# Kernel tuning notes

Measured on AMD Instinct MI355X. Metric: run time of the kernel, lower is better.

## Reference

```python
import jax, jax.numpy as jnp
from jax import lax
import numpy as np

VAR0, VAR1 = 0.1, 0.2
K_TOP, T1, T2 = 5, 0.35, 0.5
ALPHA, GAMMA, BETA = 0.25, 2.0, 0.11


def point_form(b):
    # center form (cx,cy,w,h) -> corner form (x1,y1,x2,y2)
    return jnp.concatenate([b[:, :2] - b[:, 2:] / 2, b[:, :2] + b[:, 2:] / 2], axis=-1)


def jaccard(a, b):
    # a: [N,4], b: [P,4] corner boxes -> IoU [N,P]
    lt = jnp.maximum(a[:, None, :2], b[None, :, :2])
    rb = jnp.minimum(a[:, None, 2:], b[None, :, 2:])
    wh = jnp.clip(rb - lt, 0.0)
    inter = wh[..., 0] * wh[..., 1]
    area_a = ((a[:, 2] - a[:, 0]) * (a[:, 3] - a[:, 1]))[:, None]
    area_b = ((b[:, 2] - b[:, 0]) * (b[:, 3] - b[:, 1]))[None, :]
    return inter / (area_a + area_b - inter)


def encode(matched, priors):
    # matched: corner boxes [P,4], priors: center form [P,4]
    g_cxcy = ((matched[:, :2] + matched[:, 2:]) / 2 - priors[:, :2]) / (VAR0 * priors[:, 2:])
    g_wh = jnp.log((matched[:, 2:] - matched[:, :2]) / priors[:, 2:]) / VAR1
    return jnp.concatenate([g_cxcy, g_wh], axis=-1)


def decode(loc, priors):
    cxcy = priors[:, :2] + loc[:, :2] * VAR0 * priors[:, 2:]
    wh = priors[:, 2:] * jnp.exp(loc[:, 2:] * VAR1)
    return jnp.concatenate([cxcy - wh / 2, cxcy + wh / 2], axis=-1)


def _bce_logits(x, t):
    return jnp.maximum(x, 0.0) - x * t + jnp.log1p(jnp.exp(-jnp.abs(x)))


def focal_loss(logits, target, f_iou=None):
    C = logits.shape[-1]
    t = target.reshape(-1, 1)
    keep = (t >= 0.0).astype(logits.dtype)
    t = jnp.maximum(t, 0.0)
    pos = jnp.sum(t > 0.0).astype(logits.dtype)
    x = jnp.take_along_axis(logits.reshape(-1, C), t.astype(jnp.int32), axis=1)
    ce = _bce_logits(x, t)
    a = t * ALPHA + (1.0 - t) * (1.0 - ALPHA)
    p = jax.nn.sigmoid(x)
    pt = jnp.where(t == 1.0, p, 1.0 - p)
    if f_iou is not None:
        a = lax.stop_gradient(f_iou.reshape(-1, 1)) * a
    loss = a * (1.0 - pt) ** GAMMA * ce * keep
    return jnp.sum(loss) / jnp.maximum(pos, 1.0)


def smoothl1_masked(pred, target, mask):
    # equals SmoothL1Loss on the masked rows: sum(elem)/num_rows
    x = jnp.abs(pred - target)
    elem = jnp.where(x >= BETA, x - 0.5 * BETA, 0.5 * x * x / BETA)
    n = jnp.sum(mask).astype(pred.dtype)
    return jnp.sum(elem * mask[..., None].astype(pred.dtype)) / jnp.maximum(n, 1.0)


def match_image(loc_pred, tgt, priors_c, priors_pt):
    N = tgt.shape[0]
    P = priors_c.shape[0]
    truths = tgt[:, :4]
    labels = tgt[:, 4]
    iou = jaccard(truths, priors_pt)  # [N,P]
    bt_score = jnp.max(iou, axis=0)
    bt_idx = jnp.argmax(iou, axis=0).astype(jnp.int32)

    def greedy(_, st):
        m, s, ix = st
        flat = jnp.argmax(m)
        j = (flat // P).astype(jnp.int32)
        i = (flat % P).astype(jnp.int32)
        v = m.ravel()[flat]
        m = m.at[j, :].set(-1.0)
        m = m.at[:, i].set(-1.0)
        return (m, s.at[i].set(v), ix.at[i].set(j))

    _, bt_score, bt_idx = lax.fori_loop(0, N, greedy, (iou, bt_score, bt_idx))

    conf_s1 = labels[bt_idx]
    conf_s1 = jnp.where(bt_score < T1, 0.0, conf_s1)
    loc_s1 = encode(truths[bt_idx], priors_c)

    decoded = decode(lax.stop_gradient(loc_pred), priors_c)
    c_iou = jaccard(truths, decoded)  # [N,P]
    c_bp_score = jnp.max(c_iou, axis=0)
    c_bp_idx = jnp.argmax(c_iou, axis=0).astype(jnp.int32)
    c_iou = c_iou * (c_iou >= T2).astype(c_iou.dtype)
    tk_s, tk_i = lax.top_k(c_iou, K_TOP)  # per-truth top-K priors
    c_score = jnp.zeros_like(c_bp_score)

    def assign(t, st):
        cbi, cs = st
        i = (t // K_TOP).astype(jnp.int32)
        j = t % K_TOP
        p = tk_i[i, j]
        s = tk_s[i, j]
        cond = (conf_s1[p] < 1.0) & (s > 0.0)
        cbi = cbi.at[p].set(jnp.where(cond, i, cbi[p]))
        cs = cs.at[p].set(jnp.where(cond, s, cs[p]))
        return (cbi, cs)

    c_bp_idx, c_score = lax.fori_loop(0, N * K_TOP, assign, (c_bp_idx, c_score))

    loc_s2 = encode(truths[c_bp_idx], priors_c)
    conf_s2 = labels[c_bp_idx]
    conf_s2 = jnp.where(c_score < T2, -1.0, conf_s2)
    ignore = (bt_score < T1) & (c_bp_score >= T2) & (c_score < T2)
    conf_s1 = jnp.where(ignore, -1.0, conf_s1)
    return conf_s1, loc_s1, conf_s2, loc_s2, c_score


def setup_inputs() -> dict:
    key = jax.random.key(0)
    k1, k2, k3, k4, k5, k6 = jax.random.split(key, 6)
    B, P, N, C = 16, 102400, 32, 2
    loc_data = jax.random.normal(k1, (B, P, 4), jnp.float32)
    conf_data = jax.random.normal(k2, (B, P, C), jnp.float32)
    pcxy = jax.random.uniform(k3, (P, 2), jnp.float32, 0.0, 1.0)
    pwh = jax.random.uniform(k4, (P, 2), jnp.float32, 0.02, 0.25)
    priors = jnp.concatenate([pcxy, pwh], axis=-1)
    tcxy = jax.random.uniform(k5, (B, N, 2), jnp.float32, 0.1, 0.9)
    twh = jax.random.uniform(k6, (B, N, 2), jnp.float32, 0.05, 0.3)
    x1 = jnp.clip(tcxy - twh / 2, 0.0, 1.0)
    x2 = jnp.clip(tcxy + twh / 2, 0.0, 1.0)
    targets = jnp.concatenate([x1, x2, jnp.ones((B, N, 1), jnp.float32)], axis=-1)
    return {"loc_data": loc_data, "conf_data": conf_data, "priors": priors, "targets": targets}


def reference(loc_data, conf_data, priors, targets):
    priors_c = lax.stop_gradient(priors)  # torch uses priors.data
    tgts = lax.stop_gradient(targets)     # torch uses targets[idx].data
    priors_pt = point_form(priors_c)
    conf_t, loc_t, cconf_t, cloc_t, cc_score = jax.vmap(
        lambda lp, tg: match_image(lp, tg, priors_c, priors_pt))(loc_data, tgts)
    m1 = conf_t > 0.0
    m2 = cconf_t > 0.0
    n1 = jnp.sum(m1)
    n2 = jnp.sum(m2)
    l1 = smoothl1_masked(loc_data, loc_t, m1)
    l2 = smoothl1_masked(loc_data, cloc_t, m2)
    f1 = focal_loss(conf_data, conf_t, None)
    f2 = focal_loss(conf_data, cconf_t, cc_score)
    loc_loss = jnp.where(n1 > 0, l1, 0.0) + jnp.where(n2 > 0, l2, 0.0)
    cls_loss = jnp.where(n1 > 0, f1, 0.0) + jnp.where(n2 > 0, f2, 0.0)
    none_ = (n1 == 0) & (n2 == 0)
    return (jnp.where(none_, 1e-4, loc_loss), jnp.where(none_, 1e-4, cls_loss))
```

## Files before the change

### kernel.cpp

```cpp
#include <hip/hip_runtime.h>
#include <cstdint>
#include <cstddef>

#define VAR0_ 0.1f
#define VAR1_ 0.2f
#define KTOP_ 5
#define T1_ 0.35f
#define T2_ 0.5f
#define ALPHA_ 0.25f
#define BETA_ 0.11f
#define BS 256
#define RSPLIT 8
#define ILP 4

__device__ __forceinline__ float sl1(float d) {
    float x = fabsf(d);
    return (x >= BETA_) ? (x - 0.5f * BETA_) : (0.5f * x * x / BETA_);
}

__global__ void k_init(int* __restrict__ cand_cnt, int nCnt) {
    int i = blockIdx.x * blockDim.x + threadIdx.x;
    if (i < nCnt) cand_cnt[i] = 0;
}

__global__ void k_per_prior(const float4* __restrict__ loc4, const float4* __restrict__ priors4,
                            const float* __restrict__ targets,
                            float4* __restrict__ recs4,
                            float* __restrict__ cand_v, int* __restrict__ cand_i,
                            int* __restrict__ cand_cnt,
                            int P, int N, int CAP) {
    int b = blockIdx.y;
    int tid = threadIdx.x;
    int base = blockIdx.x * (BS * ILP) + tid;
    __shared__ float4 tr4[64];
    __shared__ float trA[64];
    __shared__ float trT[64];
    for (int t = tid; t < N; t += BS) {
        float x1 = targets[(size_t)(b * N + t) * 5 + 0];
        float y1 = targets[(size_t)(b * N + t) * 5 + 1];
        float x2 = targets[(size_t)(b * N + t) * 5 + 2];
        float y2 = targets[(size_t)(b * N + t) * 5 + 3];
        tr4[t] = make_float4(x1, y1, x2, y2);
        float a = (x2 - x1) * (y2 - y1);
        trA[t] = a;
        trT[t] = a * 0.33330f;
    }
    __syncthreads();
    if (base >= P) return;

    int iv[ILP]; int val[ILP];
    float px1[ILP], py1[ILP], px2[ILP], py2[ILP], pa[ILP];
#pragma unroll
    for (int k = 0; k < ILP; k++) {
        int i = base + k * BS; iv[k] = i; val[k] = (i < P);
        float4 pr = val[k] ? priors4[i] : make_float4(0.f, 0.f, 1.f, 1.f);
        px1[k] = pr.x - pr.z * 0.5f; py1[k] = pr.y - pr.w * 0.5f;
        px2[k] = pr.x + pr.z * 0.5f; py2[k] = pr.y + pr.w * 0.5f;
        pa[k] = (px2[k] - px1[k]) * (py2[k] - py1[k]);
    }

    float bi[ILP], bu[ILP]; int bn[ILP];
#pragma unroll
    for (int k = 0; k < ILP; k++) { bi[k] = -1.f; bu[k] = 1.f; bn[k] = 0; }
#pragma unroll 2
    for (int n = 0; n < N; n++) {
        float4 t4 = tr4[n];
        float ta = trA[n];
#pragma unroll
        for (int k = 0; k < ILP; k++) {
            float lx = fmaxf(t4.x, px1[k]), ly = fmaxf(t4.y, py1[k]);
            float rx = fminf(t4.z, px2[k]), ry = fminf(t4.w, py2[k]);
            float w = fmaxf(rx - lx, 0.f), h = fmaxf(ry - ly, 0.f);
            float inter = w * h, uni = ta + pa[k] - inter;
            bool bet = inter * bu[k] > bi[k] * uni;
            bi[k] = bet ? inter : bi[k]; bu[k] = bet ? uni : bu[k]; bn[k] = bet ? n : bn[k];
        }
    }
    float bv[ILP];
#pragma unroll
    for (int k = 0; k < ILP; k++) bv[k] = bi[k] / bu[k];

    float dx1[ILP], dy1[ILP], dx2[ILP], dy2[ILP], da[ILP], daC[ILP];
#pragma unroll
    for (int k = 0; k < ILP; k++) {
        float4 pr = val[k] ? priors4[iv[k]] : make_float4(0.f, 0.f, 1.f, 1.f);
        float4 lc = val[k] ? loc4[(size_t)b * P + iv[k]] : make_float4(0.f, 0.f, 0.f, 0.f);
        float dcx = pr.x + lc.x * VAR0_ * pr.z;
        float dcy = pr.y + lc.y * VAR0_ * pr.w;
        float dw = pr.z * expf(lc.z * VAR1_);
        float dh = pr.w * expf(lc.w * VAR1_);
        dx1[k] = dcx - dw * 0.5f; dy1[k] = dcy - dh * 0.5f;
        dx2[k] = dcx + dw * 0.5f; dy2[k] = dcy + dh * 0.5f;
        da[k] = (dx2[k] - dx1[k]) * (dy2[k] - dy1[k]);
        daC[k] = da[k] * 0.33330f;
    }
    unsigned long long hm[ILP];
#pragma unroll
    for (int k = 0; k < ILP; k++) hm[k] = 0ull;
#pragma unroll 2
    for (int n = 0; n < N; n++) {
        float4 t4 = tr4[n];
        float tt = trT[n];
#pragma unroll
        for (int k = 0; k < ILP; k++) {
            float lx = fmaxf(t4.x, dx1[k]), ly = fmaxf(t4.y, dy1[k]);
            float rx = fminf(t4.z, dx2[k]), ry = fminf(t4.w, dy2[k]);
            float w = fmaxf(rx - lx, 0.f), h = fmaxf(ry - ly, 0.f);
            float inter = w * h;
            if (inter >= tt + daC[k]) hm[k] |= (1ull << n);
        }
    }

#pragma unroll
    for (int k = 0; k < ILP; k++) {
        if (!val[k]) continue;
        int had = 0;
        unsigned long long m = hm[k];
        while (m) {
            int n = __ffsll((long long)m) - 1;
            m &= m - 1;
            float4 t4 = tr4[n];
            float lx = fmaxf(t4.x, dx1[k]), ly = fmaxf(t4.y, dy1[k]);
            float rx = fminf(t4.z, dx2[k]), ry = fminf(t4.w, dy2[k]);
            float w = fmaxf(rx - lx, 0.f), h = fmaxf(ry - ly, 0.f);
            float inter = w * h;
            float v = inter / (trA[n] + da[k] - inter);
            if (v >= T2_) {
                had = 1;
                int pos = atomicAdd(&cand_cnt[b * N + n], 1);
                if (pos < CAP) {
                    size_t o = (size_t)(b * N + n) * CAP + pos;
                    cand_v[o] = v; cand_i[o] = iv[k];
                }
            }
        }
        recs4[(size_t)b * P + iv[k]] =
            make_float4(bv[k], __int_as_float(bn[k] | (had << 16)), __int_as_float(0), 0.f);
    }
}

__global__ void k_row_max_part(const float4* __restrict__ priors4, const float* __restrict__ targets,
                               float* __restrict__ part_max, int* __restrict__ part_arg,
                               int P, int N) {
    int n = blockIdx.x, b = blockIdx.y, s = blockIdx.z;
    int chunk = (P + RSPLIT - 1) / RSPLIT;
    int i0 = s * chunk;
    int i1 = min(P, i0 + chunk);
    float tx1 = targets[(size_t)(b * N + n) * 5 + 0];
    float ty1 = targets[(size_t)(b * N + n) * 5 + 1];
    float tx2 = targets[(size_t)(b * N + n) * 5 + 2];
    float ty2 = targets[(size_t)(b * N + n) * 5 + 3];
    float ta = (tx2 - tx1) * (ty2 - ty1);
    float cI[4], cU[4]; int cX[4];
#pragma unroll
    for (int k = 0; k < 4; k++) { cI[k] = -1.f; cU[k] = 1.f; cX[k] = 0x7fffffff; }
    int i = i0 + threadIdx.x;
    for (; i + 3 * BS < i1; i += 4 * BS) {
#pragma unroll
        for (int k = 0; k < 4; k++) {
            int j = i + k * BS;
            float4 pr = priors4[j];
            float px1 = pr.x - pr.z * 0.5f, py1 = pr.y - pr.w * 0.5f;
            float px2 = pr.x + pr.z * 0.5f, py2 = pr.y + pr.w * 0.5f;
            float lx = fmaxf(tx1, px1), ly = fmaxf(ty1, py1);
            float rx = fminf(tx2, px2), ry = fminf(ty2, py2);
            float w = fmaxf(rx - lx, 0.f), h = fmaxf(ry - ly, 0.f);
            float inter = w * h;
            float uni = ta + (px2 - px1) * (py2 - py1) - inter;
            bool bet = inter * cU[k] > cI[k] * uni;
            cI[k] = bet ? inter : cI[k]; cU[k] = bet ? uni : cU[k]; cX[k] = bet ? j : cX[k];
        }
    }
    for (; i < i1; i += BS) {
        float4 pr = priors4[i];
        float px1 = pr.x - pr.z * 0.5f, py1 = pr.y - pr.w * 0.5f;
        float px2 = pr.x + pr.z * 0.5f, py2 = pr.y + pr.w * 0.5f;
        float lx = fmaxf(tx1, px1), ly = fmaxf(ty1, py1);
        float rx = fminf(tx2, px2), ry = fminf(ty2, py2);
        float w = fmaxf(rx - lx, 0.f), h = fmaxf(ry - ly, 0.f);
        float inter = w * h;
        float uni = ta + (px2 - px1) * (py2 - py1) - inter;
        bool bet = inter * cU[0] > cI[0] * uni;
        cI[0] = bet ? inter : cI[0]; cU[0] = bet ? uni : cU[0]; cX[0] = bet ? i : cX[0];
    }
#pragma unroll
    for (int k = 1; k < 4; k++) {
        float l = cI[k] * cU[0], r = cI[0] * cU[k];
        bool bet = (l > r) || ((l == r) && (cX[k] < cX[0]));
        cI[0] = bet ? cI[k] : cI[0]; cU[0] = bet ? cU[k] : cU[0]; cX[0] = bet ? cX[k] : cX[0];
    }
    float bv = cI[0] / cU[0];
    int bx = cX[0];
    int tid = threadIdx.x;
    int lane = tid & 63, wid = tid >> 6;
#pragma unroll
    for (int off = 32; off > 0; off >>= 1) {
        float ov = __shfl_xor(bv, off);
        int oi = __shfl_xor(bx, off);
        if (ov > bv || (ov == bv && oi < bx)) { bv = ov; bx = oi; }
    }
    __shared__ float swv[BS / 64];
    __shared__ int swi[BS / 64];
    if (lane == 0) { swv[wid] = bv; swi[wid] = bx; }
    __syncthreads();
    if (tid == 0) {
        float fv = swv[0]; int fi = swi[0];
        for (int wv = 1; wv < BS / 64; wv++) {
            if (swv[wv] > fv || (swv[wv] == fv && swi[wv] < fi)) { fv = swv[wv]; fi = swi[wv]; }
        }
        int o = (b * N + n) * RSPLIT + s;
        part_max[o] = fv; part_arg[o] = fi;
    }
}

__global__ void k_greedy(const float4* __restrict__ priors4, const float* __restrict__ targets,
                         const float* __restrict__ part_max, const int* __restrict__ part_arg,
                         float* __restrict__ recs, int P, int N) {
    int b = blockIdx.x;
    int lane = threadIdx.x;
    extern __shared__ unsigned int mask[];
    int maskWords = (P + 31) >> 5;
    for (int w = lane; w < maskWords; w += 64) mask[w] = 0u;

    float rmax = -2.f; int rarg = 0x7fffffff; int alive = 0;
    float tx1 = 0.f, ty1 = 0.f, tx2 = 0.f, ty2 = 0.f, ta = 0.f;
    if (lane < N) {
        float bv = -2.f; int bi = 0x7fffffff;
        for (int s = 0; s < RSPLIT; s++) {
            int o = (b * N + lane) * RSPLIT + s;
            float v = part_max[o]; int ix = part_arg[o];
            if (v > bv || (v == bv && ix < bi)) { bv = v; bi = ix; }
        }
        rmax = bv; rarg = bi;
        alive = 1;
        tx1 = targets[(size_t)(b * N + lane) * 5 + 0];
        ty1 = targets[(size_t)(b * N + lane) * 5 + 1];
        tx2 = targets[(size_t)(b * N + lane) * 5 + 2];
        ty2 = targets[(size_t)(b * N + lane) * 5 + 3];
        ta = (tx2 - tx1) * (ty2 - ty1);
    }
    __syncthreads();

    for (int it = 0; it < N; it++) {
        float v = (lane < N && alive) ? rmax : -3.f;
        int idx = lane;
#pragma unroll
        for (int off = 32; off > 0; off >>= 1) {
            float ov = __shfl_xor(v, off);
            int oi = __shfl_xor(idx, off);
            if (ov > v || (ov == v && oi < idx)) { v = ov; idx = oi; }
        }
        int bj = idx;
        float bv = v;
        int sel = __shfl(rarg, bj);
        if (lane == bj) alive = 0;
        if (lane == 0) {
            float* base = recs + 4 * ((size_t)b * P + sel);
            int wrd = __float_as_int(base[1]);
            base[0] = bv;
            base[1] = __int_as_float((wrd & ~0xFFFF) | bj);
            mask[sel >> 5] |= (1u << (sel & 31));
        }
        __syncthreads();

        unsigned long long coll = __ballot(lane < N && alive && rarg == sel);
        while (coll) {
            int r = __ffsll((long long)coll) - 1;
            coll &= coll - 1;
            float rx1 = __shfl(tx1, r), ry1 = __shfl(ty1, r);
            float rx2 = __shfl(tx2, r), ry2 = __shfl(ty2, r);
            float ra = __shfl(ta, r);
            float n_i = -2.f, n_u = 1.f; int ni = 0x7fffffff;
            for (int i = lane; i < P; i += 64) {
                if (mask[i >> 5] & (1u << (i & 31))) continue;
                float4 pr = priors4[i];
                float px1 = pr.x - pr.z * 0.5f, py1 = pr.y - pr.w * 0.5f;
                float px2 = pr.x + pr.z * 0.5f, py2 = pr.y + pr.w * 0.5f;
                float lx = fmaxf(rx1, px1), ly = fmaxf(ry1, py1);
                float rx = fminf(rx2, px2), ry = fminf(ry2, py2);
                float w = fmaxf(rx - lx, 0.f), h = fmaxf(ry - ly, 0.f);
                float inter = w * h;
                float uni = ra + (px2 - px1) * (py2 - py1) - inter;
                bool better = inter * n_u > n_i * uni;
                n_i = better ? inter : n_i; n_u = better ? uni : n_u; ni = better ? i : ni;
            }
            float nv = n_i / n_u;
#pragma unroll
            for (int off = 32; off > 0; off >>= 1) {
                float ov = __shfl_xor(nv, off);
                int oi = __shfl_xor(ni, off);
                if (ov > nv || (ov == nv && oi < ni)) { nv = ov; ni = oi; }
            }
            if (lane == r) { rmax = nv; rarg = ni; }
        }
        __syncthreads();
    }
}

__global__ void k_topk(const float4* __restrict__ loc4, const float4* __restrict__ priors4,
                       const float* __restrict__ targets,
                       const float* __restrict__ cand_v, const int* __restrict__ cand_i,
                       const int* __restrict__ cand_cnt,
                       float* __restrict__ tk_s, int* __restrict__ tk_i,
                       int P, int N, int CAP) {
    int n = blockIdx.x, b = blockIdx.y;
    int row = b * N + n;
    int tid = threadIdx.x;

    float vals[KTOP_]; int ids[KTOP_];
#pragma unroll
    for (int k = 0; k < KTOP_; k++) { vals[k] = -1.f; ids[k] = 0x7fffffff; }

    int cnt = cand_cnt[row];
    if (cnt <= CAP) {
        for (int k = tid; k < cnt; k += blockDim.x) {
            float cv = cand_v[(size_t)row * CAP + k];
            int ci = cand_i[(size_t)row * CAP + k];
#pragma unroll
            for (int q = 0; q < KTOP_; q++) {
                bool better = (cv > vals[q]) || ((cv == vals[q]) && (ci < ids[q]));
                float tv = better ? cv : vals[q]; int ti = better ? ci : ids[q];
                cv = better ? vals[q] : cv; ci = better ? ids[q] : ci;
                vals[q] = tv; ids[q] = ti;
            }
        }
    } else {
        float tx1 = targets[(size_t)row * 5 + 0], ty1 = targets[(size_t)row * 5 + 1];
        float tx2 = targets[(size_t)row * 5 + 2], ty2 = targets[(size_t)row * 5 + 3];
        float ta = (tx2 - tx1) * (ty2 - ty1);
        for (int i = tid; i < P; i += blockDim.x) {
            float4 pr = priors4[i];
            size_t bp = (size_t)b * P + i;
            float4 lc = loc4[bp];
            float dcx = pr.x + lc.x * VAR0_ * pr.z;
            float dcy = pr.y + lc.y * VAR0_ * pr.w;
            float dw = pr.z * expf(lc.z * VAR1_);
            float dh = pr.w * expf(lc.w * VAR1_);
            float dx1 = dcx - dw * 0.5f, dy1 = dcy - dh * 0.5f;
            float dx2 = dcx + dw * 0.5f, dy2 = dcy + dh * 0.5f;
            float lx = fmaxf(tx1, dx1), ly = fmaxf(ty1, dy1);
            float rx = fminf(tx2, dx2), ry = fminf(ty2, dy2);
            float w = fmaxf(rx - lx, 0.f), h = fmaxf(ry - ly, 0.f);
            float inter = w * h;
            float uni = ta + (dx2 - dx1) * (dy2 - dy1) - inter;
            if (inter >= uni * 0.4999990f) {
                float v = inter / uni;
                if (v >= T2_) {
                    float cv = v; int ci = i;
#pragma unroll
                    for (int q = 0; q < KTOP_; q++) {
                        bool better = (cv > vals[q]) || ((cv == vals[q]) && (ci < ids[q]));
                        float tv = better ? cv : vals[q]; int ti = better ? ci : ids[q];
                        cv = better ? vals[q] : cv; ci = better ? ids[q] : ci;
                        vals[q] = tv; ids[q] = ti;
                    }
                }
            }
        }
    }

    __shared__ float mv[BS * KTOP_];
    __shared__ int mi[BS * KTOP_];
#pragma unroll
    for (int k = 0; k < KTOP_; k++) { mv[tid * KTOP_ + k] = vals[k]; mi[tid * KTOP_ + k] = ids[k]; }
    __syncthreads();
    for (int s = BS / 2; s > 0; s >>= 1) {
        if (tid < s) {
#pragma unroll
            for (int j = 0; j < KTOP_; j++) {
                float cv = mv[(tid + s) * KTOP_ + j];
                int ci = mi[(tid + s) * KTOP_ + j];
#pragma unroll
                for (int q = 0; q < KTOP_; q++) {
                    bool better = (cv > vals[q]) || ((cv == vals[q]) && (ci < ids[q]));
                    float tv = better ? cv : vals[q]; int ti = better ? ci : ids[q];
                    cv = better ? vals[q] : cv; ci = better ? ids[q] : ci;
                    vals[q] = tv; ids[q] = ti;
                }
            }
#pragma unroll
            for (int k = 0; k < KTOP_; k++) { mv[tid * KTOP_ + k] = vals[k]; mi[tid * KTOP_ + k] = ids[k]; }
        }
        __syncthreads();
    }
    if (tid == 0) {
#pragma unroll
        for (int k = 0; k < KTOP_; k++) {
            tk_s[(size_t)row * KTOP_ + k] = (vals[k] > 0.f) ? vals[k] : 0.f;
            tk_i[(size_t)row * KTOP_ + k] = (ids[k] == 0x7fffffff) ? 0 : ids[k];
        }
    }
}

__global__ void k_assign(const float* __restrict__ targets,
                         const float* __restrict__ tk_s, const int* __restrict__ tk_i,
                         float* __restrict__ recs, int P, int N) {
    int b = blockIdx.x;
    int tid = threadIdx.x;
    int T = N * KTOP_;
    __shared__ int sh_p[512];
    __shared__ float sh_s[512];
    __shared__ int sh_c[512];
    if (tid < T) {
        int i = tid / KTOP_, j = tid % KTOP_;
        int p = tk_i[(size_t)(b * N + i) * KTOP_ + j];
        float s = tk_s[(size_t)(b * N + i) * KTOP_ + j];
        const float* base = recs + 4 * ((size_t)b * P + p);
        float bs = base[0];
        int bj = __float_as_int(base[1]) & 0xFFFF;
        float conf1 = (bs < T1_) ? 0.f : targets[(size_t)(b * N + bj) * 5 + 4];
        sh_p[tid] = p; sh_s[tid] = s;
        sh_c[tid] = (conf1 < 1.f && s > 0.f) ? 1 : 0;
    }
    __syncthreads();
    if (tid < T && sh_c[tid]) {
        int p = sh_p[tid];
        bool last = true;
        for (int t2 = tid + 1; t2 < T; t2++) {
            if (sh_c[t2] && sh_p[t2] == p) { last = false; break; }
        }
        if (last) {
            float* base = recs + 4 * ((size_t)b * P + p);
            base[2] = __int_as_float(tid / KTOP_);
            base[3] = sh_s[tid];
        }
    }
}

__global__ void k_loss(const float4* __restrict__ loc4, const float* __restrict__ conf,
                       const float4* __restrict__ priors4, const float* __restrict__ targets,
                       const float4* __restrict__ recs4,
                       double* __restrict__ partials,
                       int P, int N, int C) {
    int b = blockIdx.y;
    int i = blockIdx.x * blockDim.x + threadIdx.x;
    double l1 = 0.0, l2 = 0.0, f1 = 0.0, f2 = 0.0;
    int n1 = 0, n2 = 0;
    if (i < P) {
        size_t bp = (size_t)b * P + i;
        float4 r = recs4[bp];
        float bs = r.x;
        int widx = __float_as_int(r.y);
        int bj = widx & 0xFFFF;
        int hadCand = (widx >> 16) & 1;
        float cs = r.w;
        int cj = (cs > 0.f) ? __float_as_int(r.z) : 0;
        float lab1 = targets[(size_t)(b * N + bj) * 5 + 4];
        float conf1 = (bs < T1_) ? 0.f : lab1;
        if ((bs < T1_) && hadCand && (cs < T2_)) conf1 = -1.f;
        float lab2 = targets[(size_t)(b * N + cj) * 5 + 4];
        float conf2 = (cs < T2_) ? -1.f : lab2;
        bool m1 = conf1 > 0.f, m2 = conf2 > 0.f;
        n1 = m1 ? 1 : 0; n2 = m2 ? 1 : 0;

        float4 pr = priors4[i];
        float pcx = pr.x, pcy = pr.y, pw = pr.z, ph = pr.w;
        float4 lc = loc4[bp];
        float p0 = lc.x, p1 = lc.y, p2 = lc.z, p3 = lc.w;

        if (m1) {
            const float* tb = &targets[(size_t)(b * N + bj) * 5];
            float gx = ((tb[0] + tb[2]) * 0.5f - pcx) / (VAR0_ * pw);
            float gy = ((tb[1] + tb[3]) * 0.5f - pcy) / (VAR0_ * ph);
            float gw = logf((tb[2] - tb[0]) / pw) / VAR1_;
            float gh = logf((tb[3] - tb[1]) / ph) / VAR1_;
            l1 = (double)(sl1(p0 - gx) + sl1(p1 - gy) + sl1(p2 - gw) + sl1(p3 - gh));
        }
        if (m2) {
            const float* tb = &targets[(size_t)(b * N + cj) * 5];
            float gx = ((tb[0] + tb[2]) * 0.5f - pcx) / (VAR0_ * pw);
            float gy = ((tb[1] + tb[3]) * 0.5f - pcy) / (VAR0_ * ph);
            float gw = logf((tb[2] - tb[0]) / pw) / VAR1_;
            float gh = logf((tb[3] - tb[1]) / ph) / VAR1_;
            l2 = (double)(sl1(p0 - gx) + sl1(p1 - gy) + sl1(p2 - gw) + sl1(p3 - gh));
        }
        float x0, x1v;
        if (C == 2) {
            float2 cv2 = ((const float2*)conf)[bp];
            x0 = cv2.x; x1v = cv2.y;
        } else {
            x0 = conf[bp * C + 0]; x1v = conf[bp * C + 1];
        }
        {
            float t = fmaxf(conf1, 0.f);
            float keep = (conf1 >= 0.f) ? 1.f : 0.f;
            float x = (t >= 1.f) ? x1v : x0;
            float ce = fmaxf(x, 0.f) - x * t + log1pf(expf(-fabsf(x)));
            float a = t * ALPHA_ + (1.f - t) * (1.f - ALPHA_);
            float pr_ = 1.f / (1.f + expf(-x));
            float pt = (t == 1.f) ? pr_ : (1.f - pr_);
            float om = 1.f - pt;
            f1 = (double)(a * om * om * ce * keep);
        }
        {
            float t = fmaxf(conf2, 0.f);
            float keep = (conf2 >= 0.f) ? 1.f : 0.f;
            float x = (t >= 1.f) ? x1v : x0;
            float ce = fmaxf(x, 0.f) - x * t + log1pf(expf(-fabsf(x)));
            float a = cs * (t * ALPHA_ + (1.f - t) * (1.f - ALPHA_));
            float pr_ = 1.f / (1.f + expf(-x));
            float pt = (t == 1.f) ? pr_ : (1.f - pr_);
            float om = 1.f - pt;
            f2 = (double)(a * om * om * ce * keep);
        }
    }
    int tid = threadIdx.x;
    int lane = tid & 63, wid = tid >> 6;
#pragma unroll
    for (int off = 32; off > 0; off >>= 1) {
        l1 += __shfl_xor(l1, off);
        l2 += __shfl_xor(l2, off);
        f1 += __shfl_xor(f1, off);
        f2 += __shfl_xor(f2, off);
        n1 += __shfl_xor(n1, off);
        n2 += __shfl_xor(n2, off);
    }
    __shared__ double swd[BS / 64][4];
    __shared__ int swn[BS / 64][2];
    if (lane == 0) {
        swd[wid][0] = l1; swd[wid][1] = l2; swd[wid][2] = f1; swd[wid][3] = f2;
        swn[wid][0] = n1; swn[wid][1] = n2;
    }
    __syncthreads();
    if (tid == 0) {
        double a0 = 0, a1 = 0, a2 = 0, a3 = 0; int b0 = 0, b1 = 0;
        for (int wv = 0; wv < BS / 64; wv++) {
            a0 += swd[wv][0]; a1 += swd[wv][1]; a2 += swd[wv][2]; a3 += swd[wv][3];
            b0 += swn[wv][0]; b1 += swn[wv][1];
        }
        int blk = blockIdx.y * gridDim.x + blockIdx.x;
        partials[(size_t)blk * 6 + 0] = a0;
        partials[(size_t)blk * 6 + 1] = a1;
        partials[(size_t)blk * 6 + 2] = a2;
        partials[(size_t)blk * 6 + 3] = a3;
        partials[(size_t)blk * 6 + 4] = (double)b0;
        partials[(size_t)blk * 6 + 5] = (double)b1;
    }
}

__global__ void k_final(const double* __restrict__ partials, int nPart, float* __restrict__ out) {
    int tid = threadIdx.x;
    double a[6] = {0, 0, 0, 0, 0, 0};
    for (int k = tid; k < nPart; k += BS) {
#pragma unroll
        for (int j = 0; j < 6; j++) a[j] += partials[(size_t)k * 6 + j];
    }
    __shared__ double sd[BS * 6];
#pragma unroll
    for (int j = 0; j < 6; j++) sd[tid * 6 + j] = a[j];
    __syncthreads();
    for (int s = BS / 2; s > 0; s >>= 1) {
        if (tid < s) {
#pragma unroll
            for (int j = 0; j < 6; j++) sd[tid * 6 + j] += sd[(tid + s) * 6 + j];
        }
        __syncthreads();
    }
    if (tid == 0) {
        double L1 = sd[0], L2 = sd[1], F1 = sd[2], F2 = sd[3], N1 = sd[4], N2 = sd[5];
        double l1v = L1 / fmax(N1, 1.0), l2v = L2 / fmax(N2, 1.0);
        double f1v = F1 / fmax(N1, 1.0), f2v = F2 / fmax(N2, 1.0);
        double locl = (N1 > 0 ? l1v : 0.0) + (N2 > 0 ? l2v : 0.0);
        double clsl = (N1 > 0 ? f1v : 0.0) + (N2 > 0 ? f2v : 0.0);
        if (N1 == 0 && N2 == 0) { locl = 1e-4; clsl = 1e-4; }
        out[0] = (float)locl;
        out[1] = (float)clsl;
    }
}

extern "C" void kernel_launch(void* const* d_in, const int* in_sizes, int n_in,
                              void* d_out, int out_size, void* d_ws, size_t ws_size,
                              hipStream_t stream) {
    const float* targets = (const float*)d_in[3];
    const float* conf = (const float*)d_in[1];
    const float4* loc4 = (const float4*)d_in[0];
    const float4* priors4 = (const float4*)d_in[2];

    int P = in_sizes[2] / 4;
    int B = in_sizes[0] / (P * 4);
    int N = in_sizes[3] / (B * 5);
    int C = in_sizes[1] / (B * P);
    const int CAP = 2048;
    size_t BP = (size_t)B * P;

    unsigned char* ws = (unsigned char*)d_ws;
    size_t off = 0;
    auto alloc = [&](size_t bytes) { size_t cur = off; off += (bytes + 255) & ~(size_t)255; return cur; };
    float* recs = (float*)(ws + alloc(BP * 16));
    float* part_max = (float*)(ws + alloc((size_t)B * N * RSPLIT * 4));
    int* part_arg = (int*)(ws + alloc((size_t)B * N * RSPLIT * 4));
    float* tk_s = (float*)(ws + alloc((size_t)B * N * KTOP_ * 4));
    int* tk_i = (int*)(ws + alloc((size_t)B * N * KTOP_ * 4));
    float* cand_v = (float*)(ws + alloc((size_t)B * N * CAP * 4));
    int* cand_i = (int*)(ws + alloc((size_t)B * N * CAP * 4));
    int* cand_cnt = (int*)(ws + alloc((size_t)B * N * 4));
    int bx = (P + BS - 1) / BS;
    double* partials = (double*)(ws + alloc((size_t)bx * B * 6 * 8));
    float* out = (float*)d_out;

    k_init<<<dim3((B * N + BS - 1) / BS), dim3(BS), 0, stream>>>(cand_cnt, B * N);
    int bx4 = (P + BS * ILP - 1) / (BS * ILP);
    k_per_prior<<<dim3(bx4, B), BS, 0, stream>>>(loc4, priors4, targets, (float4*)recs,
                                                 cand_v, cand_i, cand_cnt, P, N, CAP);
    k_row_max_part<<<dim3(N, B, RSPLIT), BS, 0, stream>>>(priors4, targets,
                                                          part_max, part_arg, P, N);
    int maskWords = (P + 31) / 32;
    size_t shmem = (size_t)maskWords * 4;
    k_greedy<<<dim3(B), 64, shmem, stream>>>(priors4, targets, part_max, part_arg,
                                             recs, P, N);
    k_topk<<<dim3(N, B), BS, 0, stream>>>(loc4, priors4, targets, cand_v, cand_i, cand_cnt,
                                          tk_s, tk_i, P, N, CAP);
    k_assign<<<dim3(B), BS, 0, stream>>>(targets, tk_s, tk_i, recs, P, N);
    k_loss<<<dim3(bx, B), BS, 0, stream>>>(loc4, conf, priors4, targets, (const float4*)recs,
                                           partials, P, N, C);
    k_final<<<1, BS, 0, stream>>>(partials, bx * B, out);
}
```

Baseline: 221.7 us.

## Process four targets per block in row-max and retune launch sizes

The row-max kernel now has each block handle four ground-truth targets over a prior chunk, so every prior load is reused across four IoU computations. The prior split grows from 8 to 16. The per-prior kernel moves to 128-thread blocks to launch more blocks. The init kernel is replaced by hipMemsetAsync, and the loss kernel only loads priors and loc when a row is positive. Together these cut redundant prior reads and launch overhead, at the cost of more registers per thread and a serialized four-step reduction with extra barriers.

```diff
diff --git a/kernel.cpp b/kernel.cpp
--- a/kernel.cpp
+++ b/kernel.cpp
@@ -10,17 +10,13 @@
 #define ALPHA_ 0.25f
 #define BETA_ 0.11f
 #define BS 256
-#define RSPLIT 8
+#define BSK 128
+#define NSPLIT 16
 #define ILP 4
 
 __device__ __forceinline__ float sl1(float d) {
     float x = fabsf(d);
     return (x >= BETA_) ? (x - 0.5f * BETA_) : (0.5f * x * x / BETA_);
-}
-
-__global__ void k_init(int* __restrict__ cand_cnt, int nCnt) {
-    int i = blockIdx.x * blockDim.x + threadIdx.x;
-    if (i < nCnt) cand_cnt[i] = 0;
 }
 
 __global__ void k_per_prior(const float4* __restrict__ loc4, const float4* __restrict__ priors4,
@@ -31,11 +27,11 @@
                             int P, int N, int CAP) {
     int b = blockIdx.y;
     int tid = threadIdx.x;
-    int base = blockIdx.x * (BS * ILP) + tid;
+    int base = blockIdx.x * (BSK * ILP) + tid;
     __shared__ float4 tr4[64];
     __shared__ float trA[64];
     __shared__ float trT[64];
-    for (int t = tid; t < N; t += BS) {
+    for (int t = tid; t < N; t += BSK) {
         float x1 = targets[(size_t)(b * N + t) * 5 + 0];
         float y1 = targets[(size_t)(b * N + t) * 5 + 1];
         float x2 = targets[(size_t)(b * N + t) * 5 + 2];
@@ -52,7 +48,7 @@
     float px1[ILP], py1[ILP], px2[ILP], py2[ILP], pa[ILP];
 #pragma unroll
     for (int k = 0; k < ILP; k++) {
-        int i = base + k * BS; iv[k] = i; val[k] = (i < P);
+        int i = base + k * BSK; iv[k] = i; val[k] = (i < P);
         float4 pr = val[k] ? priors4[i] : make_float4(0.f, 0.f, 1.f, 1.f);
         px1[k] = pr.x - pr.z * 0.5f; py1[k] = pr.y - pr.w * 0.5f;
         px2[k] = pr.x + pr.z * 0.5f; py2[k] = pr.y + pr.w * 0.5f;
@@ -142,74 +138,66 @@
 __global__ void k_row_max_part(const float4* __restrict__ priors4, const float* __restrict__ targets,
                                float* __restrict__ part_max, int* __restrict__ part_arg,
                                int P, int N) {
-    int n = blockIdx.x, b = blockIdx.y, s = blockIdx.z;
-    int chunk = (P + RSPLIT - 1) / RSPLIT;
+    int s = blockIdx.x, b = blockIdx.y, g = blockIdx.z;
+    int n0 = g * 4;
+    int chunk = (P + NSPLIT - 1) / NSPLIT;
     int i0 = s * chunk;
     int i1 = min(P, i0 + chunk);
-    float tx1 = targets[(size_t)(b * N + n) * 5 + 0];
-    float ty1 = targets[(size_t)(b * N + n) * 5 + 1];
-    float tx2 = targets[(size_t)(b * N + n) * 5 + 2];
-    float ty2 = targets[(size_t)(b * N + n) * 5 + 3];
-    float ta = (tx2 - tx1) * (ty2 - ty1);
+    float tx1[4], ty1[4], tx2[4], ty2[4], ta[4];
+#pragma unroll
+    for (int k = 0; k < 4; k++) {
+        int n = min(n0 + k, N - 1);
+        tx1[k] = targets[(size_t)(b * N + n) * 5 + 0];
+        ty1[k] = targets[(size_t)(b * N + n) * 5 + 1];
+        tx2[k] = targets[(size_t)(b * N + n) * 5 + 2];
+        ty2[k] = targets[(size_t)(b * N + n) * 5 + 3];
+        ta[k] = (tx2[k] - tx1[k]) * (ty2[k] - ty1[k]);
+    }
     float cI[4], cU[4]; int cX[4];
 #pragma unroll
     for (int k = 0; k < 4; k++) { cI[k] = -1.f; cU[k] = 1.f; cX[k] = 0x7fffffff; }
-    int i = i0 + threadIdx.x;
-    for (; i + 3 * BS < i1; i += 4 * BS) {
-#pragma unroll
-        for (int k = 0; k < 4; k++) {
-            int j = i + k * BS;
-            float4 pr = priors4[j];
-            float px1 = pr.x - pr.z * 0.5f, py1 = pr.y - pr.w * 0.5f;
-            float px2 = pr.x + pr.z * 0.5f, py2 = pr.y + pr.w * 0.5f;
-            float lx = fmaxf(tx1, px1), ly = fmaxf(ty1, py1);
-            float rx = fminf(tx2, px2), ry = fminf(ty2, py2);
-            float w = fmaxf(rx - lx, 0.f), h = fmaxf(ry - ly, 0.f);
-            float inter = w * h;
-            float uni = ta + (px2 - px1) * (py2 - py1) - inter;
-            bool bet = inter * cU[k] > cI[k] * uni;
-            cI[k] = bet ? inter : cI[k]; cU[k] = bet ? uni : cU[k]; cX[k] = bet ? j : cX[k];
-        }
-    }
-    for (; i < i1; i += BS) {
+    for (int i = i0 + threadIdx.x; i < i1; i += BS) {
         float4 pr = priors4[i];
         float px1 = pr.x - pr.z * 0.5f, py1 = pr.y - pr.w * 0.5f;
         float px2 = pr.x + pr.z * 0.5f, py2 = pr.y + pr.w * 0.5f;
-        float lx = fmaxf(tx1, px1), ly = fmaxf(ty1, py1);
-        float rx = fminf(tx2, px2), ry = fminf(ty2, py2);
-        float w = fmaxf(rx - lx, 0.f), h = fmaxf(ry - ly, 0.f);
-        float inter = w * h;
-        float uni = ta + (px2 - px1) * (py2 - py1) - inter;
-        bool bet = inter * cU[0] > cI[0] * uni;
-        cI[0] = bet ? inter : cI[0]; cU[0] = bet ? uni : cU[0]; cX[0] = bet ? i : cX[0];
-    }
-#pragma unroll
-    for (int k = 1; k < 4; k++) {
-        float l = cI[k] * cU[0], r = cI[0] * cU[k];
-        bool bet = (l > r) || ((l == r) && (cX[k] < cX[0]));
-        cI[0] = bet ? cI[k] : cI[0]; cU[0] = bet ? cU[k] : cU[0]; cX[0] = bet ? cX[k] : cX[0];
-    }
-    float bv = cI[0] / cU[0];
-    int bx = cX[0];
+        float pa = (px2 - px1) * (py2 - py1);
+#pragma unroll
+        for (int k = 0; k < 4; k++) {
+            float lx = fmaxf(tx1[k], px1), ly = fmaxf(ty1[k], py1);
+            float rx = fminf(tx2[k], px2), ry = fminf(ty2[k], py2);
+            float w = fmaxf(rx - lx, 0.f), h = fmaxf(ry - ly, 0.f);
+            float inter = w * h;
+            float uni = ta[k] + pa - inter;
+            bool bet = inter * cU[k] > cI[k] * uni;
+            cI[k] = bet ? inter : cI[k]; cU[k] = bet ? uni : cU[k]; cX[k] = bet ? i : cX[k];
+        }
+    }
     int tid = threadIdx.x;
     int lane = tid & 63, wid = tid >> 6;
-#pragma unroll
-    for (int off = 32; off > 0; off >>= 1) {
-        float ov = __shfl_xor(bv, off);
-        int oi = __shfl_xor(bx, off);
-        if (ov > bv || (ov == bv && oi < bx)) { bv = ov; bx = oi; }
-    }
     __shared__ float swv[BS / 64];
     __shared__ int swi[BS / 64];
-    if (lane == 0) { swv[wid] = bv; swi[wid] = bx; }
-    __syncthreads();
-    if (tid == 0) {
-        float fv = swv[0]; int fi = swi[0];
-        for (int wv = 1; wv < BS / 64; wv++) {
-            if (swv[wv] > fv || (swv[wv] == fv && swi[wv] < fi)) { fv = swv[wv]; fi = swi[wv]; }
-        }
-        int o = (b * N + n) * RSPLIT + s;
-        part_max[o] = fv; part_arg[o] = fi;
+#pragma unroll
+    for (int k = 0; k < 4; k++) {
+        if (n0 + k >= N) break;
+        float bv = cI[k] / cU[k];
+        int bx = cX[k];
+#pragma unroll
+        for (int off = 32; off > 0; off >>= 1) {
+            float ov = __shfl_xor(bv, off);
+            int oi = __shfl_xor(bx, off);
+            if (ov > bv || (ov == bv && oi < bx)) { bv = ov; bx = oi; }
+        }
+        if (lane == 0) { swv[wid] = bv; swi[wid] = bx; }
+        __syncthreads();
+        if (tid == 0) {
+            float fv = swv[0]; int fi = swi[0];
+            for (int wv = 1; wv < BS / 64; wv++) {
+                if (swv[wv] > fv || (swv[wv] == fv && swi[wv] < fi)) { fv = swv[wv]; fi = swi[wv]; }
+            }
+            int o = (b * N + (n0 + k)) * NSPLIT + s;
+            part_max[o] = fv; part_arg[o] = fi;
+        }
+        __syncthreads();
     }
 }
 
@@ -226,8 +214,8 @@
     float tx1 = 0.f, ty1 = 0.f, tx2 = 0.f, ty2 = 0.f, ta = 0.f;
     if (lane < N) {
         float bv = -2.f; int bi = 0x7fffffff;
-        for (int s = 0; s < RSPLIT; s++) {
-            int o = (b * N + lane) * RSPLIT + s;
+        for (int s = 0; s < NSPLIT; s++) {
+            int o = (b * N + lane) * NSPLIT + s;
             float v = part_max[o]; int ix = part_arg[o];
             if (v > bv || (v == bv && ix < bi)) { bv = v; bi = ix; }
         }
@@ -453,26 +441,27 @@
         bool m1 = conf1 > 0.f, m2 = conf2 > 0.f;
         n1 = m1 ? 1 : 0; n2 = m2 ? 1 : 0;
 
-        float4 pr = priors4[i];
-        float pcx = pr.x, pcy = pr.y, pw = pr.z, ph = pr.w;
-        float4 lc = loc4[bp];
-        float p0 = lc.x, p1 = lc.y, p2 = lc.z, p3 = lc.w;
-
-        if (m1) {
-            const float* tb = &targets[(size_t)(b * N + bj) * 5];
-            float gx = ((tb[0] + tb[2]) * 0.5f - pcx) / (VAR0_ * pw);
-            float gy = ((tb[1] + tb[3]) * 0.5f - pcy) / (VAR0_ * ph);
-            float gw = logf((tb[2] - tb[0]) / pw) / VAR1_;
-            float gh = logf((tb[3] - tb[1]) / ph) / VAR1_;
-            l1 = (double)(sl1(p0 - gx) + sl1(p1 - gy) + sl1(p2 - gw) + sl1(p3 - gh));
-        }
-        if (m2) {
-            const float* tb = &targets[(size_t)(b * N + cj) * 5];
-            float gx = ((tb[0] + tb[2]) * 0.5f - pcx) / (VAR0_ * pw);
-            float gy = ((tb[1] + tb[3]) * 0.5f - pcy) / (VAR0_ * ph);
-            float gw = logf((tb[2] - tb[0]) / pw) / VAR1_;
-            float gh = logf((tb[3] - tb[1]) / ph) / VAR1_;
-            l2 = (double)(sl1(p0 - gx) + sl1(p1 - gy) + sl1(p2 - gw) + sl1(p3 - gh));
+        if (m1 || m2) {
+            float4 pr = priors4[i];
+            float pcx = pr.x, pcy = pr.y, pw = pr.z, ph = pr.w;
+            float4 lc = loc4[bp];
+            float p0 = lc.x, p1 = lc.y, p2 = lc.z, p3 = lc.w;
+            if (m1) {
+                const float* tb = &targets[(size_t)(b * N + bj) * 5];
+                float gx = ((tb[0] + tb[2]) * 0.5f - pcx) / (VAR0_ * pw);
+                float gy = ((tb[1] + tb[3]) * 0.5f - pcy) / (VAR0_ * ph);
+                float gw = logf((tb[2] - tb[0]) / pw) / VAR1_;
+                float gh = logf((tb[3] - tb[1]) / ph) / VAR1_;
+                l1 = (double)(sl1(p0 - gx) + sl1(p1 - gy) + sl1(p2 - gw) + sl1(p3 - gh));
+            }
+            if (m2) {
+                const float* tb = &targets[(size_t)(b * N + cj) * 5];
+                float gx = ((tb[0] + tb[2]) * 0.5f - pcx) / (VAR0_ * pw);
+                float gy = ((tb[1] + tb[3]) * 0.5f - pcy) / (VAR0_ * ph);
+                float gw = logf((tb[2] - tb[0]) / pw) / VAR1_;
+                float gh = logf((tb[3] - tb[1]) / ph) / VAR1_;
+                l2 = (double)(sl1(p0 - gx) + sl1(p1 - gy) + sl1(p2 - gw) + sl1(p3 - gh));
+            }
         }
         float x0, x1v;
         if (C == 2) {
@@ -587,8 +576,8 @@
     size_t off = 0;
     auto alloc = [&](size_t bytes) { size_t cur = off; off += (bytes + 255) & ~(size_t)255; return cur; };
     float* recs = (float*)(ws + alloc(BP * 16));
-    float* part_max = (float*)(ws + alloc((size_t)B * N * RSPLIT * 4));
-    int* part_arg = (int*)(ws + alloc((size_t)B * N * RSPLIT * 4));
+    float* part_max = (float*)(ws + alloc((size_t)B * N * NSPLIT * 4));
+    int* part_arg = (int*)(ws + alloc((size_t)B * N * NSPLIT * 4));
     float* tk_s = (float*)(ws + alloc((size_t)B * N * KTOP_ * 4));
     int* tk_i = (int*)(ws + alloc((size_t)B * N * KTOP_ * 4));
     float* cand_v = (float*)(ws + alloc((size_t)B * N * CAP * 4));
@@ -598,12 +587,13 @@
     double* partials = (double*)(ws + alloc((size_t)bx * B * 6 * 8));
     float* out = (float*)d_out;
 
-    k_init<<<dim3((B * N + BS - 1) / BS), dim3(BS), 0, stream>>>(cand_cnt, B * N);
-    int bx4 = (P + BS * ILP - 1) / (BS * ILP);
-    k_per_prior<<<dim3(bx4, B), BS, 0, stream>>>(loc4, priors4, targets, (float4*)recs,
-                                                 cand_v, cand_i, cand_cnt, P, N, CAP);
-    k_row_max_part<<<dim3(N, B, RSPLIT), BS, 0, stream>>>(priors4, targets,
-                                                          part_max, part_arg, P, N);
+    hipMemsetAsync(cand_cnt, 0, (size_t)B * N * 4, stream);
+    int bx4 = (P + BSK * ILP - 1) / (BSK * ILP);
+    k_per_prior<<<dim3(bx4, B), BSK, 0, stream>>>(loc4, priors4, targets, (float4*)recs,
+                                                  cand_v, cand_i, cand_cnt, P, N, CAP);
+    int ngroup = (N + 3) / 4;
+    k_row_max_part<<<dim3(NSPLIT, B, ngroup), BS, 0, stream>>>(priors4, targets,
+                                                               part_max, part_arg, P, N);
     int maskWords = (P + 31) / 32;
     size_t shmem = (size_t)maskWords * 4;
     k_greedy<<<dim3(B), 64, shmem, stream>>>(priors4, targets, part_max, part_arg,
```

Result: faster. 213.6 us (-3.7%).
